# Kernel optimization log

Measured on AMD Instinct MI355X. Metric: run time of the kernel, lower is better.

## Reference

```python
import jax, jax.numpy as jnp
import numpy as np
from jax import lax

B, NUM_E, NUM_R, H, C, K = 8192, 20000, 500, 512, 50, 3
EPS = 1e-5


def batchnorm(x, g, b, axes, shape):
    # training-mode BN: biased batch statistics (matches torch default forward)
    m = jnp.mean(x, axis=axes, keepdims=True)
    v = jnp.var(x, axis=axes, keepdims=True)
    return (x - m) / jnp.sqrt(v + EPS) * g.reshape(shape) + b.reshape(shape)


def setup_inputs() -> dict:
    key = jax.random.key(0)
    ks = jax.random.split(key, 12)
    facts = jax.random.randint(ks[0], (B, 3), 0, NUM_R)
    ent_emb = jax.random.normal(ks[1], (NUM_E, H), jnp.float32)
    rel_emb = jax.random.normal(ks[2], (NUM_R, H), jnp.float32)
    e_r_bias = jax.random.normal(ks[3], (NUM_E, H), jnp.float32)
    conv_w = jax.random.normal(ks[4], (C, 3, K), jnp.float32) * (1.0 / np.sqrt(3 * K))
    conv_b = jnp.zeros((C,), jnp.float32)
    fc_w = jax.random.normal(ks[5], (H, H * C), jnp.float32) * (1.0 / np.sqrt(H * C))
    fc_b = jnp.zeros((H,), jnp.float32)
    bn0_g = jnp.ones((3,), jnp.float32); bn0_b = jnp.zeros((3,), jnp.float32)
    bn1_g = jnp.ones((C,), jnp.float32); bn1_b = jnp.zeros((C,), jnp.float32)
    bn2_g = jnp.ones((H,), jnp.float32); bn2_b = jnp.zeros((H,), jnp.float32)
    return {"facts": facts, "ent_emb": ent_emb, "rel_emb": rel_emb, "e_r_bias": e_r_bias,
            "conv_w": conv_w, "conv_b": conv_b, "fc_w": fc_w, "fc_b": fc_b,
            "bn0_g": bn0_g, "bn0_b": bn0_b, "bn1_g": bn1_g, "bn1_b": bn1_b,
            "bn2_g": bn2_g, "bn2_b": bn2_b}


def reference(facts, ent_emb, rel_emb, e_r_bias, conv_w, conv_b, fc_w, fc_b,
              bn0_g, bn0_b, bn1_g, bn1_b, bn2_g, bn2_b):
    e_s = ent_emb[facts[:, 0]]        # (B, H)
    e_r = rel_emb[facts[:, 1]]        # (B, H)
    bias = e_r_bias[facts[:, 0]]      # (B, H)
    x = jnp.stack([e_s, e_r, bias], axis=1)            # (B, 3, H)
    x = batchnorm(x, bn0_g, bn0_b, (0, 2), (1, 3, 1))  # BatchNorm1d(3)
    pad = K // 2
    x = lax.conv_general_dilated(x, conv_w, window_strides=(1,),
                                 padding=((pad, pad),),
                                 dimension_numbers=("NCH", "OIH", "NCH"))
    x = x + conv_b[None, :, None]                      # (B, C, H)
    x = batchnorm(x, bn1_g, bn1_b, (0, 2), (1, C, 1))  # BatchNorm1d(C)
    x = jax.nn.relu(x)
    x = x.reshape(B, C * H)
    x = x @ fc_w.T + fc_b                              # (B, H)
    x = batchnorm(x, bn2_g, bn2_b, (0,), (1, H))       # BatchNorm1d(H), len>1
    x = jax.nn.relu(x)
    score = x @ ent_emb.T                              # (B, NUM_E)
    # F.softmax then log == log_softmax
    return jax.nn.log_softmax(score, axis=-1)
```

## Files before the change

kernel.cpp:

```cpp
#include <hip/hip_runtime.h>

#define B_SZ   8192
#define NUM_E  20000
#define H_DIM  512
#define C_DIM  50
#define KHW    25600
#define EPS    1e-5f
#define KSPLIT 8
#define NBLK   157

typedef short bf16x8 __attribute__((ext_vector_type(8)));
typedef float f32x4  __attribute__((ext_vector_type(4)));

__device__ __forceinline__ float bf2f(unsigned short u) {
  return __uint_as_float(((unsigned int)u) << 16);
}
__device__ __forceinline__ unsigned short f2bf(float f) {
  unsigned int u = __float_as_uint(f);
  return (unsigned short)((u + 0x7FFFu + ((u >> 16) & 1u)) >> 16);
}

__global__ __launch_bounds__(256) void cvt_bf16_kernel(const float* __restrict__ in,
                                                       unsigned short* __restrict__ out,
                                                       int n4) {
  int i = blockIdx.x * 256 + threadIdx.x;
  int stride = gridDim.x * 256;
  for (; i < n4; i += stride) {
    float4 v = reinterpret_cast<const float4*>(in)[i];
    ushort4 o;
    o.x = f2bf(v.x); o.y = f2bf(v.y); o.z = f2bf(v.z); o.w = f2bf(v.w);
    reinterpret_cast<ushort4*>(out)[i] = o;
  }
}

__global__ __launch_bounds__(256) void bn0_stats_kernel(const int* __restrict__ facts,
                                                        const float* __restrict__ ent,
                                                        const float* __restrict__ rel,
                                                        const float* __restrict__ bias,
                                                        float* __restrict__ stats) {
  const int tid = threadIdx.x;
  float s0=0.f,s1=0.f,s2=0.f,q0=0.f,q1=0.f,q2=0.f;
  const int stride = gridDim.x * 256;
  for (int i = blockIdx.x * 256 + tid; i < B_SZ * H_DIM; i += stride) {
    int b = i >> 9, h = i & 511;
    int f0 = facts[b * 3 + 0], f1 = facts[b * 3 + 1];
    float v0 = ent[f0 * H_DIM + h];
    float v1 = rel[f1 * H_DIM + h];
    float v2 = bias[f0 * H_DIM + h];
    s0 += v0; q0 += v0 * v0;
    s1 += v1; q1 += v1 * v1;
    s2 += v2; q2 += v2 * v2;
  }
  __shared__ float red[256];
  float vals[6] = {s0, s1, s2, q0, q1, q2};
  for (int j = 0; j < 6; ++j) {
    red[tid] = vals[j]; __syncthreads();
    for (int off = 128; off > 0; off >>= 1) {
      if (tid < off) red[tid] += red[tid + off];
      __syncthreads();
    }
    if (tid == 0) atomicAdd(&stats[j], red[0]);
    __syncthreads();
  }
}

__global__ __launch_bounds__(256) void xn_kernel(const int* __restrict__ facts,
                                                 const float* __restrict__ ent,
                                                 const float* __restrict__ rel,
                                                 const float* __restrict__ bias,
                                                 const float* __restrict__ g0,
                                                 const float* __restrict__ b0,
                                                 const float* __restrict__ stats,
                                                 unsigned short* __restrict__ xn) {
  const float invN = 1.0f / 4194304.0f;
  float a[3], c[3];
  #pragma unroll
  for (int ch = 0; ch < 3; ++ch) {
    float mean = stats[ch] * invN;
    float var  = stats[3 + ch] * invN - mean * mean;
    float sc = g0[ch] * rsqrtf(var + EPS);
    a[ch] = sc;
    c[ch] = b0[ch] - mean * sc;
  }
  const int stride = gridDim.x * 256;
  for (int i = blockIdx.x * 256 + threadIdx.x; i < B_SZ * H_DIM; i += stride) {
    int b = i >> 9, h = i & 511;
    int f0 = facts[b * 3 + 0], f1 = facts[b * 3 + 1];
    xn[(b * 3 + 0) * H_DIM + h] = f2bf(fmaf(ent[f0 * H_DIM + h],  a[0], c[0]));
    xn[(b * 3 + 1) * H_DIM + h] = f2bf(fmaf(rel[f1 * H_DIM + h],  a[1], c[1]));
    xn[(b * 3 + 2) * H_DIM + h] = f2bf(fmaf(bias[f0 * H_DIM + h], a[2], c[2]));
  }
}

__global__ __launch_bounds__(256) void conv_stats_kernel(const unsigned short* __restrict__ xn,
                                                         const float* __restrict__ conv_w,
                                                         const float* __restrict__ conv_b,
                                                         float* __restrict__ stats) {
  const int tid = threadIdx.x;
  const int cg = blockIdx.y;
  float w[8][9], cb[8];
  #pragma unroll
  for (int j = 0; j < 8; ++j) {
    int c = cg * 8 + j;
    if (c < C_DIM) {
      #pragma unroll
      for (int t = 0; t < 9; ++t) w[j][t] = conv_w[c * 9 + t];
      cb[j] = conv_b[c];
    } else {
      #pragma unroll
      for (int t = 0; t < 9; ++t) w[j][t] = 0.f;
      cb[j] = 0.f;
    }
  }
  float s[8], qv[8];
  #pragma unroll
  for (int j = 0; j < 8; ++j) { s[j] = 0.f; qv[j] = 0.f; }
  const int stride = gridDim.x * 256;
  for (int i = blockIdx.x * 256 + tid; i < B_SZ * H_DIM; i += stride) {
    int b = i >> 9, h = i & 511;
    float xv[9];
    #pragma unroll
    for (int ii = 0; ii < 3; ++ii) {
      const unsigned short* row = xn + ((size_t)b * 3 + ii) * H_DIM;
      xv[ii * 3 + 0] = (h > 0)   ? bf2f(row[h - 1]) : 0.f;
      xv[ii * 3 + 1] = bf2f(row[h]);
      xv[ii * 3 + 2] = (h < 511) ? bf2f(row[h + 1]) : 0.f;
    }
    #pragma unroll
    for (int j = 0; j < 8; ++j) {
      float v = cb[j];
      #pragma unroll
      for (int t = 0; t < 9; ++t) v = fmaf(w[j][t], xv[t], v);
      s[j] += v; qv[j] += v * v;
    }
  }
  __shared__ float red[256];
  #pragma unroll 1
  for (int j = 0; j < 8; ++j) {
    int c = cg * 8 + j;
    red[tid] = s[j]; __syncthreads();
    for (int off = 128; off > 0; off >>= 1) {
      if (tid < off) red[tid] += red[tid + off];
      __syncthreads();
    }
    if (tid == 0 && c < C_DIM) atomicAdd(&stats[8 + c], red[0]);
    __syncthreads();
    red[tid] = qv[j]; __syncthreads();
    for (int off = 128; off > 0; off >>= 1) {
      if (tid < off) red[tid] += red[tid + off];
      __syncthreads();
    }
    if (tid == 0 && c < C_DIM) atomicAdd(&stats[64 + c], red[0]);
    __syncthreads();
  }
}

__global__ __launch_bounds__(64) void bn1_fold_kernel(const float* __restrict__ conv_w,
                                                      const float* __restrict__ conv_b,
                                                      const float* __restrict__ g1,
                                                      const float* __restrict__ b1,
                                                      const float* __restrict__ stats,
                                                      float* __restrict__ cwf) {
  const int c = threadIdx.x;
  if (c >= C_DIM) return;
  const float invN = 1.0f / 4194304.0f;
  float mean = stats[8 + c] * invN;
  float var  = stats[64 + c] * invN - mean * mean;
  float sc = g1[c] * rsqrtf(var + EPS);
  float tc = fmaf(sc, conv_b[c], b1[c] - mean * sc);
  #pragma unroll
  for (int t = 0; t < 9; ++t) cwf[c * 10 + t] = conv_w[c * 9 + t] * sc;
  cwf[c * 10 + 9] = tc;
}

__global__ __launch_bounds__(512) void fc_gemm_kernel(const unsigned short* __restrict__ xn,
                                                      const unsigned short* __restrict__ fcw,
                                                      const float* __restrict__ cwf,
                                                      float* __restrict__ z) {
  const int tid  = threadIdx.x;
  const int m0   = blockIdx.x * 128;
  const int hs   = blockIdx.y * 64;
  const int lane = tid & 63;
  const int wave = tid >> 6;
  const int wm   = (wave >> 2) * 64;
  const int wn   = (wave & 3) * 128;
  const int l15  = lane & 15;
  const int qd   = lane >> 4;
  const int am   = tid >> 2;
  const int ah   = (tid & 3) * 8;

  __shared__ unsigned short xstage[128][3][36];
  __shared__ unsigned short albuf[2][128][40];

  f32x4 acc[4][8];
  #pragma unroll
  for (int a = 0; a < 4; ++a)
    #pragma unroll
    for (int b = 0; b < 8; ++b) {
      f32x4 zv = {0.f, 0.f, 0.f, 0.f};
      acc[a][b] = zv;
    }

  const unsigned short* bbase[8];
  #pragma unroll
  for (int tn = 0; tn < 8; ++tn)
    bbase[tn] = fcw + (size_t)(wn + tn * 16 + l15) * KHW + qd * 8;

  float xw[3][10];

  for (int h0 = hs; h0 < hs + 64; h0 += 32) {
    __syncthreads();
    for (int idx = tid; idx < 128 * 3 * 34; idx += 512) {
      int m = idx / 102;
      int rem = idx - m * 102;
      int i = rem / 34;
      int x = rem - i * 34;
      int h = h0 - 1 + x;
      unsigned short v = 0;
      if (h >= 0 && h < H_DIM) v = xn[((size_t)(m0 + m) * 3 + i) * H_DIM + h];
      xstage[m][i][x] = v;
    }
    __syncthreads();
    #pragma unroll
    for (int i = 0; i < 3; ++i) {
      const unsigned int* p = (const unsigned int*)&xstage[am][i][ah];
      #pragma unroll
      for (int j = 0; j < 5; ++j) {
        unsigned int u = p[j];
        xw[i][2 * j]     = __uint_as_float(u << 16);
        xw[i][2 * j + 1] = __uint_as_float(u & 0xFFFF0000u);
      }
    }

    auto agen = [&](int c, int bb) {
      float w[9], tc;
      const float* cw = cwf + c * 10;
      #pragma unroll
      for (int t = 0; t < 9; ++t) w[t] = cw[t];
      tc = cw[9];
      unsigned int pk[4];
      #pragma unroll
      for (int kp = 0; kp < 4; ++kp) {
        float vv[2];
        #pragma unroll
        for (int e = 0; e < 2; ++e) {
          int kk = kp * 2 + e;
          float v = tc;
          #pragma unroll
          for (int i = 0; i < 3; ++i) {
            v = fmaf(w[i * 3 + 0], xw[i][kk],     v);
            v = fmaf(w[i * 3 + 1], xw[i][kk + 1], v);
            v = fmaf(w[i * 3 + 2], xw[i][kk + 2], v);
          }
          vv[e] = fmaxf(v, 0.f);
        }
        asm("v_cvt_pk_bf16_f32 %0, %1, %2" : "=v"(pk[kp]) : "v"(vv[0]), "v"(vv[1]));
      }
      *(uint4*)&albuf[bb][am][ah] = make_uint4(pk[0], pk[1], pk[2], pk[3]);
    };

    agen(0, 0);
    bf16x8 bcur[8];
    #pragma unroll
    for (int tn = 0; tn < 8; ++tn)
      bcur[tn] = *(const bf16x8*)(bbase[tn] + h0);
    __syncthreads();

    #pragma unroll 1
    for (int c = 0; c < C_DIM; ++c) {
      bf16x8 af[4];
      #pragma unroll
      for (int tm = 0; tm < 4; ++tm)
        af[tm] = *(const bf16x8*)&albuf[c & 1][wm + tm * 16 + l15][qd * 8];
      #pragma unroll
      for (int tm = 0; tm < 4; ++tm)
        #pragma unroll
        for (int tn = 0; tn < 8; ++tn)
          acc[tm][tn] = __builtin_amdgcn_mfma_f32_16x16x32_bf16(af[tm], bcur[tn], acc[tm][tn], 0, 0, 0);
      if (c + 1 < C_DIM) {
        bf16x8 bnew[8];
        #pragma unroll
        for (int tn = 0; tn < 8; ++tn)
          bnew[tn] = *(const bf16x8*)(bbase[tn] + (c + 1) * H_DIM + h0);
        agen(c + 1, (c + 1) & 1);
        __syncthreads();
        #pragma unroll
        for (int tn = 0; tn < 8; ++tn) bcur[tn] = bnew[tn];
      } else {
        __syncthreads();
      }
    }
  }

  #pragma unroll
  for (int tm = 0; tm < 4; ++tm)
    #pragma unroll
    for (int tn = 0; tn < 8; ++tn) {
      int col = wn + tn * 16 + l15;
      #pragma unroll
      for (int r = 0; r < 4; ++r) {
        int row = m0 + wm + tm * 16 + qd * 4 + r;
        atomicAdd(&z[(size_t)row * H_DIM + col], acc[tm][tn][r]);
      }
    }
}

__global__ __launch_bounds__(256) void bn2_stats_kernel(const float* __restrict__ z,
                                                        float* __restrict__ stats) {
  const int tid = threadIdx.x;
  const int col = blockIdx.y * 64 + (tid & 63);
  float s = 0.f, qq = 0.f;
  for (int r = blockIdx.x * 4 + (tid >> 6); r < B_SZ; r += gridDim.x * 4) {
    float v = z[(size_t)r * H_DIM + col];
    s += v; qq += v * v;
  }
  __shared__ float ls[256], lq[256];
  ls[tid] = s; lq[tid] = qq;
  __syncthreads();
  if (tid < 64) {
    s  = ls[tid] + ls[tid + 64] + ls[tid + 128] + ls[tid + 192];
    qq = lq[tid] + lq[tid + 64] + lq[tid + 128] + lq[tid + 192];
    atomicAdd(&stats[128 + col], s);
    atomicAdd(&stats[640 + col], qq);
  }
}

__global__ __launch_bounds__(256) void zr_kernel(const float* __restrict__ z,
                                                 const float* __restrict__ stats,
                                                 const float* __restrict__ g2,
                                                 const float* __restrict__ b2,
                                                 unsigned short* __restrict__ zrb) {
  const float invB = 1.0f / 8192.0f;
  const int stride = gridDim.x * 256;
  for (int i = blockIdx.x * 256 + threadIdx.x; i < B_SZ * H_DIM; i += stride) {
    int col = i & 511;
    float mean = stats[128 + col] * invB;
    float var  = stats[640 + col] * invB - mean * mean;
    float sc = g2[col] * rsqrtf(var + EPS);
    float tc = b2[col] - mean * sc;
    float v = fmaf(z[i], sc, tc);
    zrb[i] = f2bf(fmaxf(v, 0.f));
  }
}

__global__ __launch_bounds__(256) void score_gemm_kernel(const unsigned short* __restrict__ zrb,
                                                         const unsigned short* __restrict__ entb,
                                                         float* __restrict__ out,
                                                         float* __restrict__ pm,
                                                         float* __restrict__ ps) {
  const int tid  = threadIdx.x;
  const int m0   = blockIdx.x * 128;
  const int n0   = blockIdx.y * 128;
  const int lane = tid & 63;
  const int wave = tid >> 6;
  const int wm   = (wave >> 1) * 64;
  const int wn   = (wave & 1) * 64;
  const int l15  = lane & 15;
  const int qd   = lane >> 4;

  f32x4 acc[4][4];
  #pragma unroll
  for (int a = 0; a < 4; ++a)
    #pragma unroll
    for (int b = 0; b < 4; ++b) {
      f32x4 zv = {0.f, 0.f, 0.f, 0.f};
      acc[a][b] = zv;
    }

  const unsigned short* ap[4];
  const unsigned short* bp[4];
  #pragma unroll
  for (int t = 0; t < 4; ++t) {
    ap[t] = zrb + (size_t)(m0 + wm + t * 16 + l15) * H_DIM + qd * 8;
    int e = n0 + wn + t * 16 + l15;
    if (e >= NUM_E) e = NUM_E - 1;
    bp[t] = entb + (size_t)e * H_DIM + qd * 8;
  }
  #pragma unroll 2
  for (int k0 = 0; k0 < H_DIM; k0 += 32) {
    bf16x8 af[4], bf[4];
    #pragma unroll
    for (int t = 0; t < 4; ++t) {
      af[t] = *(const bf16x8*)(ap[t] + k0);
      bf[t] = *(const bf16x8*)(bp[t] + k0);
    }
    #pragma unroll
    for (int tm = 0; tm < 4; ++tm)
      #pragma unroll
      for (int tn = 0; tn < 4; ++tn)
        acc[tm][tn] = __builtin_amdgcn_mfma_f32_16x16x32_bf16(af[tm], bf[tn], acc[tm][tn], 0, 0, 0);
  }
  #pragma unroll
  for (int tm = 0; tm < 4; ++tm)
    #pragma unroll
    for (int tn = 0; tn < 4; ++tn) {
      int col = n0 + wn + tn * 16 + l15;
      if (col < NUM_E) {
        #pragma unroll
        for (int r = 0; r < 4; ++r) {
          int row = m0 + wm + tm * 16 + qd * 4 + r;
          out[(size_t)row * NUM_E + col] = acc[tm][tn][r];
        }
      }
    }

  __shared__ float smx[2][2][4][4][4];
  __shared__ float ssx[2][2][4][4][4];
  const int wmb = wave >> 1, wnb = wave & 1;
  #pragma unroll
  for (int tm = 0; tm < 4; ++tm) {
    #pragma unroll
    for (int r = 0; r < 4; ++r) {
      float m = -3.0e38f;
      #pragma unroll
      for (int tn = 0; tn < 4; ++tn) {
        int col = n0 + wn + tn * 16 + l15;
        if (col < NUM_E) m = fmaxf(m, acc[tm][tn][r]);
      }
      float s = 0.f;
      #pragma unroll
      for (int tn = 0; tn < 4; ++tn) {
        int col = n0 + wn + tn * 16 + l15;
        if (col < NUM_E) s += __expf(acc[tm][tn][r] - m);
      }
      #pragma unroll
      for (int d = 1; d < 16; d <<= 1) {
        float m2 = __shfl_xor(m, d, 64);
        float s2 = __shfl_xor(s, d, 64);
        float Mn = fmaxf(m, m2);
        s = s * __expf(m - Mn) + s2 * __expf(m2 - Mn);
        m = Mn;
      }
      if (l15 == 0) { smx[wmb][wnb][tm][qd][r] = m; ssx[wmb][wnb][tm][qd][r] = s; }
    }
  }
  __syncthreads();
  if (tid < 128) {
    int wmb2 = tid >> 6, rl = tid & 63;
    int tm = rl >> 4, qd2 = (rl >> 2) & 3, r = rl & 3;
    float m1 = smx[wmb2][0][tm][qd2][r], s1 = ssx[wmb2][0][tm][qd2][r];
    float m2 = smx[wmb2][1][tm][qd2][r], s2 = ssx[wmb2][1][tm][qd2][r];
    float Mn = fmaxf(m1, m2);
    float S  = s1 * __expf(m1 - Mn) + s2 * __expf(m2 - Mn);
    int row  = m0 + wmb2 * 64 + rl;
    pm[(size_t)blockIdx.y * B_SZ + row] = Mn;
    ps[(size_t)blockIdx.y * B_SZ + row] = S;
  }
}

__global__ __launch_bounds__(256) void lse_reduce_kernel(const float* __restrict__ pm,
                                                         const float* __restrict__ ps,
                                                         float* __restrict__ lse) {
  int row = blockIdx.x * 256 + threadIdx.x;
  float M = -3.0e38f, S = 0.f;
  for (int nb = 0; nb < NBLK; ++nb) {
    float m2 = pm[(size_t)nb * B_SZ + row];
    float s2 = ps[(size_t)nb * B_SZ + row];
    float Mn = fmaxf(M, m2);
    S = S * __expf(M - Mn) + s2 * __expf(m2 - Mn);
    M = Mn;
  }
  lse[row] = M + __logf(S);
}

__global__ __launch_bounds__(256) void lsub_kernel(float* __restrict__ out,
                                                   const float* __restrict__ lse) {
  const int row = blockIdx.y;
  const float l = lse[row];
  float4* p = (float4*)(out + (size_t)row * NUM_E);
  int i = blockIdx.x * 256 + threadIdx.x;
  if (i < NUM_E / 4) {
    float4 v = p[i];
    v.x -= l; v.y -= l; v.z -= l; v.w -= l;
    p[i] = v;
  }
}

extern "C" void kernel_launch(void* const* d_in, const int* in_sizes, int n_in,
                              void* d_out, int out_size, void* d_ws, size_t ws_size,
                              hipStream_t stream) {
  const int*   facts  = (const int*)d_in[0];
  const float* ent    = (const float*)d_in[1];
  const float* rel    = (const float*)d_in[2];
  const float* erb    = (const float*)d_in[3];
  const float* conv_w = (const float*)d_in[4];
  const float* conv_b = (const float*)d_in[5];
  const float* fc_w   = (const float*)d_in[6];
  const float* g0     = (const float*)d_in[8];
  const float* b0     = (const float*)d_in[9];
  const float* g1     = (const float*)d_in[10];
  const float* b1     = (const float*)d_in[11];
  const float* g2     = (const float*)d_in[12];
  const float* b2     = (const float*)d_in[13];

  char* ws = (char*)d_ws;
  float*          stats = (float*)ws;
  float*          cwf   = (float*)(ws + 8192);
  unsigned short* xn    = (unsigned short*)(ws + 16384);
  unsigned short* fcw   = (unsigned short*)(ws + 25182208);
  unsigned short* entb  = (unsigned short*)(ws + 51396608);
  float*          z     = (float*)(ws + 71876608);
  unsigned short* zrb   = (unsigned short*)(ws + 88653824);
  float*          pm    = (float*)(ws + 71876608);
  float*          psx   = (float*)(ws + 71876608 + 5144576);
  float*          lse   = (float*)(ws + 71876608 + 10289152);
  float* out = (float*)d_out;

  hipMemsetAsync(stats, 0, 16384, stream);
  hipMemsetAsync(z, 0, 16777216, stream);
  cvt_bf16_kernel<<<2048, 256, 0, stream>>>(ent, entb, (NUM_E * H_DIM) / 4);
  cvt_bf16_kernel<<<2048, 256, 0, stream>>>(fc_w, fcw, (H_DIM * KHW) / 4);
  bn0_stats_kernel<<<1024, 256, 0, stream>>>(facts, ent, rel, erb, stats);
  xn_kernel<<<1024, 256, 0, stream>>>(facts, ent, rel, erb, g0, b0, stats, xn);
  conv_stats_kernel<<<dim3(512, 7), 256, 0, stream>>>(xn, conv_w, conv_b, stats);
  bn1_fold_kernel<<<1, 64, 0, stream>>>(conv_w, conv_b, g1, b1, stats, cwf);
  fc_gemm_kernel<<<dim3(64, KSPLIT), 512, 0, stream>>>(xn, fcw, cwf, z);
  bn2_stats_kernel<<<dim3(64, 8), 256, 0, stream>>>(z, stats);
  zr_kernel<<<2048, 256, 0, stream>>>(z, stats, g2, b2, zrb);
  score_gemm_kernel<<<dim3(64, NBLK), 256, 0, stream>>>(zrb, entb, out, pm, psx);
  lse_reduce_kernel<<<32, 256, 0, stream>>>(pm, psx, lse);
  lsub_kernel<<<dim3(20, 8192), 256, 0, stream>>>(out, lse);
}
```

Before: 2.526 ms.

## Stage score GEMM tiles through double-buffered swizzled LDS with async global_load_lds

Replaces direct per-wave global loads of A and B fragments in the score GEMM with a double-buffered LDS pipeline. Each k-step of 64 is loaded with global_load_lds into XOR-swizzled shared tiles while the previous tile feeds the MFMAs. The goal is to share tile loads across the four waves instead of fetching redundantly, and to hide global latency behind compute. It adds 64KB of LDS per block, which may reduce occupancy, plus two barriers per iteration.

```diff
diff --git a/kernel.cpp b/kernel.cpp
--- a/kernel.cpp
+++ b/kernel.cpp
@@ -358,6 +358,9 @@
   const int l15  = lane & 15;
   const int qd   = lane >> 4;
 
+  __shared__ unsigned short As[2][128 * 64];
+  __shared__ unsigned short Bs[2][128 * 64];
+
   f32x4 acc[4][4];
   #pragma unroll
   for (int a = 0; a < 4; ++a)
@@ -367,29 +370,61 @@
       acc[a][b] = zv;
     }
 
-  const unsigned short* ap[4];
-  const unsigned short* bp[4];
-  #pragma unroll
-  for (int t = 0; t < 4; ++t) {
-    ap[t] = zrb + (size_t)(m0 + wm + t * 16 + l15) * H_DIM + qd * 8;
-    int e = n0 + wn + t * 16 + l15;
-    if (e >= NUM_E) e = NUM_E - 1;
-    bp[t] = entb + (size_t)e * H_DIM + qd * 8;
-  }
-  #pragma unroll 2
-  for (int k0 = 0; k0 < H_DIM; k0 += 32) {
-    bf16x8 af[4], bf[4];
-    #pragma unroll
-    for (int t = 0; t < 4; ++t) {
-      af[t] = *(const bf16x8*)(ap[t] + k0);
-      bf[t] = *(const bf16x8*)(bp[t] + k0);
-    }
-    #pragma unroll
-    for (int tm = 0; tm < 4; ++tm)
-      #pragma unroll
-      for (int tn = 0; tn < 4; ++tn)
-        acc[tm][tn] = __builtin_amdgcn_mfma_f32_16x16x32_bf16(af[tm], bf[tn], acc[tm][tn], 0, 0, 0);
-  }
+  auto stage = [&](const unsigned short* __restrict__ src, int row0, int maxrow,
+                   unsigned short* dst, int k0) {
+    #pragma unroll
+    for (int i = 0; i < 4; ++i) {
+      int rgrp = i * 32 + wave * 8;
+      int row  = rgrp + (lane >> 3);
+      int srow = row0 + row;
+      if (srow > maxrow) srow = maxrow;
+      int cs = (lane & 7) ^ (row & 7);
+      const unsigned short* g = src + (size_t)srow * H_DIM + k0 + cs * 8;
+      __builtin_amdgcn_global_load_lds(
+          (const __attribute__((address_space(1))) void*)g,
+          (__attribute__((address_space(3))) void*)(dst + rgrp * 64),
+          16, 0, 0);
+    }
+  };
+
+  stage(zrb,  m0, B_SZ  - 1, As[0], 0);
+  stage(entb, n0, NUM_E - 1, Bs[0], 0);
+
+  #pragma unroll 1
+  for (int t = 0; t < 8; ++t) {
+    const int cur = t & 1;
+    if (t < 7) {
+      stage(zrb,  m0, B_SZ  - 1, As[cur ^ 1], (t + 1) * 64);
+      stage(entb, n0, NUM_E - 1, Bs[cur ^ 1], (t + 1) * 64);
+      asm volatile("s_waitcnt vmcnt(8)" ::: "memory");
+    } else {
+      asm volatile("s_waitcnt vmcnt(0)" ::: "memory");
+    }
+    __builtin_amdgcn_s_barrier();
+    __builtin_amdgcn_sched_barrier(0);
+
+    const unsigned short* At = As[cur];
+    const unsigned short* Bt = Bs[cur];
+    #pragma unroll
+    for (int ks = 0; ks < 2; ++ks) {
+      bf16x8 af[4], bfr[4];
+      #pragma unroll
+      for (int f = 0; f < 4; ++f) {
+        int ra = wm + f * 16 + l15;
+        af[f]  = *(const bf16x8*)&At[ra * 64 + (((ks * 4 + qd) ^ (ra & 7)) << 3)];
+        int rb = wn + f * 16 + l15;
+        bfr[f] = *(const bf16x8*)&Bt[rb * 64 + (((ks * 4 + qd) ^ (rb & 7)) << 3)];
+      }
+      #pragma unroll
+      for (int tm = 0; tm < 4; ++tm)
+        #pragma unroll
+        for (int tn = 0; tn < 4; ++tn)
+          acc[tm][tn] = __builtin_amdgcn_mfma_f32_16x16x32_bf16(af[tm], bfr[tn], acc[tm][tn], 0, 0, 0);
+    }
+    __builtin_amdgcn_sched_barrier(0);
+    __builtin_amdgcn_s_barrier();
+  }
+
   #pragma unroll
   for (int tm = 0; tm < 4; ++tm)
     #pragma unroll
```

Result: faster. 2.236 ms (-11.5%).
